# Kernel tuning notes

Measured on AMD Instinct MI355X. Metric: run time of the kernel, lower is better.

## Reference

```python
import jax, jax.numpy as jnp
import numpy as np

N = 20000      # nodes
E = 320000     # directed edges (self-loops added inside reference)
DIN = 128      # input_dim
HID = 64       # hidden_dim
H = 4          # num_heads
B = 16         # graphs in batch
OUT = 1        # output_dim
NEG_SLOPE = 0.2


def setup_inputs() -> dict:
    key = jax.random.key(0)
    ks = jax.random.split(key, 20)
    p = lambda k, shape: (jax.random.normal(k, shape, jnp.float32) * 0.05)
    x = jax.random.normal(ks[0], (N, DIN), jnp.float32)
    edge_index = jax.random.randint(ks[1], (2, E), 0, N, dtype=jnp.int64)
    batch = jnp.sort(jax.random.randint(ks[2], (N,), 0, B, dtype=jnp.int64))
    return {
        "x": x, "edge_index": edge_index, "batch": batch,
        # gat1: DIN -> (H, HID), concat
        "W1": p(ks[3], (DIN, H * HID)), "as1": p(ks[4], (H, HID)), "ad1": p(ks[5], (H, HID)), "b1": jnp.zeros((H * HID,), jnp.float32),
        # gat2: H*HID -> (H, HID), concat
        "W2": p(ks[6], (H * HID, H * HID)), "as2": p(ks[7], (H, HID)), "ad2": p(ks[8], (H, HID)), "b2": jnp.zeros((H * HID,), jnp.float32),
        # gat_out: H*HID -> (1, HID), mean (concat=False)
        "W3": p(ks[9], (H * HID, HID)), "as3": p(ks[10], (1, HID)), "ad3": p(ks[11], (1, HID)), "b3": jnp.zeros((HID,), jnp.float32),
        "wp": p(ks[12], (HID, 1)), "bp": jnp.zeros((1,), jnp.float32),
        "wr": p(ks[13], (HID, OUT)), "br": jnp.zeros((OUT,), jnp.float32),
    }


def _gat_layer(x, W, a_src, a_dst, bias, src, dst, heads, concat):
    n = x.shape[0]
    h = (x @ W).reshape(n, heads, -1)                      # [N,H,C]
    e_src = (h * a_src).sum(-1)                            # [N,H]
    e_dst = (h * a_dst).sum(-1)                            # [N,H]
    e = jax.nn.leaky_relu(e_src[src] + e_dst[dst], NEG_SLOPE)  # [Etot,H]
    # segment softmax over destination node (self-loops guarantee non-empty)
    m = jax.ops.segment_max(e, dst, num_segments=n)
    e = jnp.exp(e - m[dst])
    den = jax.ops.segment_sum(e, dst, num_segments=n)
    alpha = e / den[dst]                                   # [Etot,H]
    out = jax.ops.segment_sum(h[src] * alpha[..., None], dst, num_segments=n)  # [N,H,C]
    out = out.reshape(n, -1) if concat else out.mean(axis=1)
    return out + bias


def reference(x, edge_index, batch, W1, as1, ad1, b1, W2, as2, ad2, b2,
              W3, as3, ad3, b3, wp, bp, wr, br):
    n = x.shape[0]
    loops = jnp.arange(n, dtype=edge_index.dtype)
    src = jnp.concatenate([edge_index[0], loops])
    dst = jnp.concatenate([edge_index[1], loops])

    h = jax.nn.elu(_gat_layer(x, W1, as1, ad1, b1, src, dst, H, True))
    h = jax.nn.elu(_gat_layer(h, W2, as2, ad2, b2, src, dst, H, True))
    h = jax.nn.elu(_gat_layer(h, W3, as3, ad3, b3, src, dst, 1, False))  # [N,HID]

    attn = jax.nn.sigmoid(h @ wp + bp)                     # [N,1]
    hw = h * attn                                          # [N,HID]
    sums = jax.ops.segment_sum(hw, batch, num_segments=B)  # [B,HID]
    counts = jax.ops.segment_sum(jnp.ones((n,), hw.dtype), batch, num_segments=B)
    pooled = sums / jnp.maximum(counts, 1.0)[:, None]
    return pooled @ wr + br                                # [B,OUT]
```

## Files before the change

### kernel.cpp

```cpp
#include <hip/hip_runtime.h>


typedef unsigned short u16;
typedef __attribute__((ext_vector_type(8))) short bf16x8;
typedef __attribute__((ext_vector_type(4))) float f32x4;

__device__ __forceinline__ u16 bf16rn(float x) {
    unsigned u = __float_as_uint(x);
    u += 0x7FFFu + ((u >> 16) & 1u);
    return (u16)(u >> 16);
}
__device__ __forceinline__ float bf16f(u16 h) {
    return __uint_as_float(((unsigned)h) << 16);
}

__device__ __forceinline__ void gload16(const u16* g, u16* l) {
    __builtin_amdgcn_global_load_lds(
        (const __attribute__((address_space(1))) unsigned int*)g,
        (__attribute__((address_space(3))) unsigned int*)l, 16, 0, 0);
}

__global__ void edge_hist_k(const int* __restrict__ ei, int E, int n, int* __restrict__ deg) {
    int i = blockIdx.x * blockDim.x + threadIdx.x;
    if (i >= E + n) return;
    int dst = (i < E) ? ei[E + i] : (i - E);
    atomicAdd(&deg[dst], 1);
}

__global__ void scan_p1_k(const int* __restrict__ deg, int* __restrict__ bsum, int n) {
    __shared__ int red[256];
    int tid = threadIdx.x;
    int i = blockIdx.x * 256 + tid;
    int v = (i < n) ? deg[i] : 0;
    red[tid] = v;
    __syncthreads();
    for (int off = 128; off; off >>= 1) {
        if (tid < off) red[tid] += red[tid + off];
        __syncthreads();
    }
    if (tid == 0) bsum[blockIdx.x] = red[0];
}

__global__ __launch_bounds__(1024) void scan_p2_k(int* __restrict__ bsum, int nb) {
    __shared__ int part[1024];
    int tid = threadIdx.x;
    int v = (tid < nb) ? bsum[tid] : 0;
    part[tid] = v;
    __syncthreads();
    for (int off = 1; off < 1024; off <<= 1) {
        int t = (tid >= off) ? part[tid - off] : 0;
        __syncthreads();
        part[tid] += t;
        __syncthreads();
    }
    if (tid < nb) bsum[tid] = part[tid] - v;
}

__global__ void scan_p3_k(const int* __restrict__ deg, const int* __restrict__ bsum,
                          int* __restrict__ rowptr, int* __restrict__ cursor, int n) {
    __shared__ int part[256];
    int tid = threadIdx.x;
    int i = blockIdx.x * 256 + tid;
    int v = (i < n) ? deg[i] : 0;
    part[tid] = v;
    __syncthreads();
    for (int off = 1; off < 256; off <<= 1) {
        int t = (tid >= off) ? part[tid - off] : 0;
        __syncthreads();
        part[tid] += t;
        __syncthreads();
    }
    int excl = part[tid] - v + bsum[blockIdx.x];
    if (i < n) { rowptr[i] = excl; cursor[i] = excl; }
    if (i == n - 1) rowptr[n] = excl + v;
}

__global__ void edge_scatter_k(const int* __restrict__ ei, int E, int n,
                               int* __restrict__ cursor, int* __restrict__ srcs) {
    int i = blockIdx.x * blockDim.x + threadIdx.x;
    if (i >= E + n) return;
    int src, dst;
    if (i < E) { src = ei[i]; dst = ei[E + i]; }
    else       { src = i - E; dst = src; }
    int pos = atomicAdd(&cursor[dst], 1);
    srcs[pos] = src;
}

__global__ void split_bf16_k(const float* __restrict__ in, u16* __restrict__ hi,
                             u16* __restrict__ lo, int n4) {
    int i = blockIdx.x * 256 + threadIdx.x;
    if (i >= n4) return;
    float4 v = reinterpret_cast<const float4*>(in)[i];
    u16 hx = bf16rn(v.x), hy = bf16rn(v.y), hz = bf16rn(v.z), hw = bf16rn(v.w);
    ushort4 H = make_ushort4(hx, hy, hz, hw);
    ushort4 L = make_ushort4(bf16rn(v.x - bf16f(hx)), bf16rn(v.y - bf16f(hy)),
                             bf16rn(v.z - bf16f(hz)), bf16rn(v.w - bf16f(hw)));
    reinterpret_cast<ushort4*>(hi)[i] = H;
    reinterpret_cast<ushort4*>(lo)[i] = L;
}

__global__ void splitT_bf16_k(const float* __restrict__ W, u16* __restrict__ thi,
                              u16* __restrict__ tlo, int K, int Nn) {
    int idx = blockIdx.x * 256 + threadIdx.x;
    if (idx >= K * Nn) return;
    int k = idx / Nn, nn = idx - k * Nn;
    float v = W[idx];
    u16 h = bf16rn(v);
    u16 l = bf16rn(v - bf16f(h));
    thi[(size_t)nn * K + k] = h;
    tlo[(size_t)nn * K + k] = l;
}

template <int NF>
__global__ __launch_bounds__(256) void gemm_lds_k(
        const u16* __restrict__ Ahi, const u16* __restrict__ Alo,
        const u16* __restrict__ Bthi, const u16* __restrict__ Btlo,
        float* __restrict__ C,
        const float* __restrict__ a_src, const float* __restrict__ a_dst,
        float* __restrict__ esrc, float* __restrict__ edst,
        int M, int Nn, int K) {
    __shared__ u16 Ah[2][4][64 * 8];
    __shared__ u16 Al[2][4][64 * 8];
    const int mb = (M + 63) >> 6;
    const int mi = blockIdx.x % mb;
    const int ni = blockIdx.x / mb;
    const int m0 = mi * 64;
    const int n0 = ni * (NF * 64);
    const int tid = threadIdx.x;
    const int wv = tid >> 6;
    const int lane = tid & 63;
    const int rr = lane & 15;
    const int kg = lane >> 4;

    int srow = m0 + lane; if (srow > M - 1) srow = M - 1;
    const u16* sh = Ahi + (size_t)srow * K + wv * 8;
    const u16* sl = Alo + (size_t)srow * K + wv * 8;

    const u16* pbh[NF];
    const u16* pbl[NF];
#pragma unroll
    for (int nf = 0; nf < NF; ++nf) {
        int col = n0 + (wv * NF + nf) * 16 + rr;
        pbh[nf] = Bthi + (size_t)col * K + kg * 8;
        pbl[nf] = Btlo + (size_t)col * K + kg * 8;
    }

    f32x4 acc[4][NF];
#pragma unroll
    for (int mf = 0; mf < 4; ++mf)
#pragma unroll
        for (int nf = 0; nf < NF; ++nf) acc[mf][nf] = (f32x4){0.f, 0.f, 0.f, 0.f};

    bf16x8 bhc[NF], blc[NF], bhn[NF], bln[NF];
#pragma unroll
    for (int nf = 0; nf < NF; ++nf) {
        bhc[nf] = *reinterpret_cast<const bf16x8*>(pbh[nf]);
        blc[nf] = *reinterpret_cast<const bf16x8*>(pbl[nf]);
    }
    gload16(sh, &Ah[0][wv][0]);
    gload16(sl, &Al[0][wv][0]);
    __syncthreads();

    const int NT = K >> 5;
    for (int t = 0; t < NT; ++t) {
        const int cur = t & 1;
        if (t + 1 < NT) {
            const int kc = (t + 1) << 5;
#pragma unroll
            for (int nf = 0; nf < NF; ++nf) {
                bhn[nf] = *reinterpret_cast<const bf16x8*>(pbh[nf] + kc);
                bln[nf] = *reinterpret_cast<const bf16x8*>(pbl[nf] + kc);
            }
            gload16(sh + kc, &Ah[cur ^ 1][wv][0]);
            gload16(sl + kc, &Al[cur ^ 1][wv][0]);
        }
        bf16x8 ah[4], al[4];
#pragma unroll
        for (int mf = 0; mf < 4; ++mf) {
            ah[mf] = *reinterpret_cast<const bf16x8*>(&Ah[cur][kg][(mf * 16 + rr) * 8]);
            al[mf] = *reinterpret_cast<const bf16x8*>(&Al[cur][kg][(mf * 16 + rr) * 8]);
        }
#pragma unroll
        for (int mf = 0; mf < 4; ++mf)
#pragma unroll
            for (int nf = 0; nf < NF; ++nf) {
                acc[mf][nf] = __builtin_amdgcn_mfma_f32_16x16x32_bf16(ah[mf], bhc[nf], acc[mf][nf], 0, 0, 0);
                acc[mf][nf] = __builtin_amdgcn_mfma_f32_16x16x32_bf16(ah[mf], blc[nf], acc[mf][nf], 0, 0, 0);
                acc[mf][nf] = __builtin_amdgcn_mfma_f32_16x16x32_bf16(al[mf], bhc[nf], acc[mf][nf], 0, 0, 0);
            }
#pragma unroll
        for (int nf = 0; nf < NF; ++nf) { bhc[nf] = bhn[nf]; blc[nf] = bln[nf]; }
        __syncthreads();
    }

#pragma unroll
    for (int mf = 0; mf < 4; ++mf)
#pragma unroll
        for (int nf = 0; nf < NF; ++nf) {
            int col = n0 + (wv * NF + nf) * 16 + rr;
            float* cb = C + ((size_t)(col >> 6) * M) * 64 + (col & 63);
#pragma unroll
            for (int rg = 0; rg < 4; ++rg) {
                int row = m0 + mf * 16 + kg * 4 + rg;
                if (row < M) cb[(size_t)row * 64] = acc[mf][nf][rg];
            }
        }

    float asv[NF], adv[NF];
#pragma unroll
    for (int nf = 0; nf < NF; ++nf) {
        int col = n0 + (wv * NF + nf) * 16 + rr;
        asv[nf] = a_src[col];
        adv[nf] = a_dst[col];
    }
    float ps[4][4], pd[4][4];
#pragma unroll
    for (int mf = 0; mf < 4; ++mf)
#pragma unroll
        for (int rg = 0; rg < 4; ++rg) {
            float s = 0.f, dvv = 0.f;
#pragma unroll
            for (int nf = 0; nf < NF; ++nf) {
                s = fmaf(acc[mf][nf][rg], asv[nf], s);
                dvv = fmaf(acc[mf][nf][rg], adv[nf], dvv);
            }
#pragma unroll
            for (int off = 1; off < 16; off <<= 1) {
                s += __shfl_xor(s, off);
                dvv += __shfl_xor(dvv, off);
            }
            ps[mf][rg] = s;
            pd[mf][rg] = dvv;
        }
    float* sm_src = (float*)&Ah[0][0][0];
    float* sm_dst = sm_src + 256;
    if (rr == 0) {
#pragma unroll
        for (int mf = 0; mf < 4; ++mf)
#pragma unroll
            for (int rg = 0; rg < 4; ++rg) {
                int rl = mf * 16 + kg * 4 + rg;
                sm_src[wv * 64 + rl] = ps[mf][rg];
                sm_dst[wv * 64 + rl] = pd[mf][rg];
            }
    }
    __syncthreads();
    if (tid < 64) {
        int row = m0 + tid;
        if (row < M) {
            const int HTOT = Nn >> 6;
            constexpr int WPH = 4 / NF;
#pragma unroll
            for (int hl = 0; hl < NF; ++hl) {
                float es = 0.f, edv = 0.f;
#pragma unroll
                for (int w = 0; w < WPH; ++w) {
                    es += sm_src[(hl * WPH + w) * 64 + tid];
                    edv += sm_dst[(hl * WPH + w) * 64 + tid];
                }
                int hg = ni * NF + hl;
                esrc[(size_t)row * HTOT + hg] = es;
                edst[(size_t)row * HTOT + hg] = edv;
            }
        }
    }
}

__global__ __launch_bounds__(256) void gat_aggregate_hm_k(
        const float* __restrict__ hm, const float* __restrict__ esrc,
        const float* __restrict__ edst, const int* __restrict__ rowptr,
        const int* __restrict__ srcs, const float* __restrict__ bias,
        u16* __restrict__ ghi, u16* __restrict__ glo, int n) {
    __shared__ int2 swb[4][64];
    int wv = threadIdx.x >> 6;
    int d = blockIdx.x * 4 + wv;
    int lane = threadIdx.x & 63;
    int hh = blockIdx.y;
    if (d >= n) return;
    const float* hbase = hm + (size_t)hh * n * 64;
    const int es = lane >> 4;
    const int cq = lane & 15;
    int2* swv = swb[wv];
    float ed = edst[d * 4 + hh];
    int lo = rowptr[d], hi = rowptr[d + 1];
    float4 acc = make_float4(0.f, 0.f, 0.f, 0.f);
    float den = 0.f;
    for (int base = lo; base < hi; base += 64) {
        int cnt = min(64, hi - base);
        int idx = base + lane;
        int s = srcs[(idx < hi) ? idx : lo];
        float e = esrc[s * 4 + hh] + ed;
        e = (e >= 0.f) ? e : 0.2f * e;
        float w = (lane < cnt) ? __expf(e) : 0.f;
        float ws = w;
#pragma unroll
        for (int off = 1; off < 64; off <<= 1) ws += __shfl_xor(ws, off);
        den += ws;
        swv[lane] = make_int2(s, __float_as_int(w));
        auto ROW = [&](int2 sv) -> float4 {
            return *reinterpret_cast<const float4*>(&hbase[(size_t)sv.x * 64 + cq * 4]);
        };
        int2 s0 = swv[es], s1 = swv[4 + es], s2 = swv[8 + es], s3 = swv[12 + es];
        float4 p0 = ROW(s0), p1 = ROW(s1), p2 = ROW(s2), p3 = ROW(s3);
        for (int j = 0; j < cnt; j += 16) {
            int2 t0 = s0, t1 = s1, t2 = s2, t3 = s3;
            float4 q0 = p0, q1 = p1, q2 = p2, q3 = p3;
            s0 = swv[(j + 16 + es) & 63];
            s1 = swv[(j + 20 + es) & 63];
            s2 = swv[(j + 24 + es) & 63];
            s3 = swv[(j + 28 + es) & 63];
            p0 = ROW(s0); p1 = ROW(s1); p2 = ROW(s2); p3 = ROW(s3);
            float w0 = __int_as_float(t0.y), w1 = __int_as_float(t1.y);
            float w2 = __int_as_float(t2.y), w3 = __int_as_float(t3.y);
            acc.x = fmaf(w0, q0.x, acc.x); acc.y = fmaf(w0, q0.y, acc.y);
            acc.z = fmaf(w0, q0.z, acc.z); acc.w = fmaf(w0, q0.w, acc.w);
            acc.x = fmaf(w1, q1.x, acc.x); acc.y = fmaf(w1, q1.y, acc.y);
            acc.z = fmaf(w1, q1.z, acc.z); acc.w = fmaf(w1, q1.w, acc.w);
            acc.x = fmaf(w2, q2.x, acc.x); acc.y = fmaf(w2, q2.y, acc.y);
            acc.z = fmaf(w2, q2.z, acc.z); acc.w = fmaf(w2, q2.w, acc.w);
            acc.x = fmaf(w3, q3.x, acc.x); acc.y = fmaf(w3, q3.y, acc.y);
            acc.z = fmaf(w3, q3.z, acc.z); acc.w = fmaf(w3, q3.w, acc.w);
        }
    }
    acc.x += __shfl_xor(acc.x, 16); acc.x += __shfl_xor(acc.x, 32);
    acc.y += __shfl_xor(acc.y, 16); acc.y += __shfl_xor(acc.y, 32);
    acc.z += __shfl_xor(acc.z, 16); acc.z += __shfl_xor(acc.z, 32);
    acc.w += __shfl_xor(acc.w, 16); acc.w += __shfl_xor(acc.w, 32);
    if (es == 0) {
        int c0 = hh * 64 + cq * 4;
        float inv = 1.f / den;
        float4 bv = *reinterpret_cast<const float4*>(&bias[c0]);
        float4 o;
        o.x = acc.x * inv + bv.x;
        o.y = acc.y * inv + bv.y;
        o.z = acc.z * inv + bv.z;
        o.w = acc.w * inv + bv.w;
        o.x = (o.x > 0.f) ? o.x : expm1f(o.x);
        o.y = (o.y > 0.f) ? o.y : expm1f(o.y);
        o.z = (o.z > 0.f) ? o.z : expm1f(o.z);
        o.w = (o.w > 0.f) ? o.w : expm1f(o.w);
        u16 hx = bf16rn(o.x), hy = bf16rn(o.y), hz = bf16rn(o.z), hw = bf16rn(o.w);
        ushort4 H = make_ushort4(hx, hy, hz, hw);
        ushort4 L = make_ushort4(bf16rn(o.x - bf16f(hx)), bf16rn(o.y - bf16f(hy)),
                                 bf16rn(o.z - bf16f(hz)), bf16rn(o.w - bf16f(hw)));
        *reinterpret_cast<ushort4*>(&ghi[(size_t)d * 256 + c0]) = H;
        *reinterpret_cast<ushort4*>(&glo[(size_t)d * 256 + c0]) = L;
    }
}

__global__ __launch_bounds__(256) void gat_aggregate1_attn_k(
        const float* __restrict__ hin, const float* __restrict__ esrc,
        const float* __restrict__ edst, const int* __restrict__ rowptr,
        const int* __restrict__ srcs, const float* __restrict__ bias,
        const float* __restrict__ wp, const float* __restrict__ bp,
        float* __restrict__ gout, float* __restrict__ attn, int n) {
    __shared__ int2 swb[4][64];
    int wv = threadIdx.x >> 6;
    int d = blockIdx.x * 4 + wv;
    int lane = threadIdx.x & 63;
    if (d >= n) return;
    const int es = lane >> 4;
    const int cq = lane & 15;
    int2* swv = swb[wv];
    float ed = edst[d];
    int lo = rowptr[d], hi = rowptr[d + 1];
    float4 acc = make_float4(0.f, 0.f, 0.f, 0.f);
    float den = 0.f;
    for (int base = lo; base < hi; base += 64) {
        int cnt = min(64, hi - base);
        int idx = base + lane;
        int s = srcs[(idx < hi) ? idx : lo];
        float e = esrc[s] + ed;
        e = (e >= 0.f) ? e : 0.2f * e;
        float w = (lane < cnt) ? __expf(e) : 0.f;
        float ws = w;
#pragma unroll
        for (int off = 1; off < 64; off <<= 1) ws += __shfl_xor(ws, off);
        den += ws;
        swv[lane] = make_int2(s, __float_as_int(w));
        auto ROW = [&](int2 sv) -> float4 {
            return *reinterpret_cast<const float4*>(&hin[(size_t)sv.x * 64 + cq * 4]);
        };
        int2 s0 = swv[es], s1 = swv[4 + es], s2 = swv[8 + es], s3 = swv[12 + es];
        float4 p0 = ROW(s0), p1 = ROW(s1), p2 = ROW(s2), p3 = ROW(s3);
        for (int j = 0; j < cnt; j += 16) {
            int2 t0 = s0, t1 = s1, t2 = s2, t3 = s3;
            float4 q0 = p0, q1 = p1, q2 = p2, q3 = p3;
            s0 = swv[(j + 16 + es) & 63];
            s1 = swv[(j + 20 + es) & 63];
            s2 = swv[(j + 24 + es) & 63];
            s3 = swv[(j + 28 + es) & 63];
            p0 = ROW(s0); p1 = ROW(s1); p2 = ROW(s2); p3 = ROW(s3);
            float w0 = __int_as_float(t0.y), w1 = __int_as_float(t1.y);
            float w2 = __int_as_float(t2.y), w3 = __int_as_float(t3.y);
            acc.x = fmaf(w0, q0.x, acc.x); acc.y = fmaf(w0, q0.y, acc.y);
            acc.z = fmaf(w0, q0.z, acc.z); acc.w = fmaf(w0, q0.w, acc.w);
            acc.x = fmaf(w1, q1.x, acc.x); acc.y = fmaf(w1, q1.y, acc.y);
            acc.z = fmaf(w1, q1.z, acc.z); acc.w = fmaf(w1, q1.w, acc.w);
            acc.x = fmaf(w2, q2.x, acc.x); acc.y = fmaf(w2, q2.y, acc.y);
            acc.z = fmaf(w2, q2.z, acc.z); acc.w = fmaf(w2, q2.w, acc.w);
            acc.x = fmaf(w3, q3.x, acc.x); acc.y = fmaf(w3, q3.y, acc.y);
            acc.z = fmaf(w3, q3.z, acc.z); acc.w = fmaf(w3, q3.w, acc.w);
        }
    }
    acc.x += __shfl_xor(acc.x, 16); acc.x += __shfl_xor(acc.x, 32);
    acc.y += __shfl_xor(acc.y, 16); acc.y += __shfl_xor(acc.y, 32);
    acc.z += __shfl_xor(acc.z, 16); acc.z += __shfl_xor(acc.z, 32);
    acc.w += __shfl_xor(acc.w, 16); acc.w += __shfl_xor(acc.w, 32);
    int c0 = cq * 4;
    float inv = 1.f / den;
    float4 bv = *reinterpret_cast<const float4*>(&bias[c0]);
    float4 o;
    o.x = acc.x * inv + bv.x;
    o.y = acc.y * inv + bv.y;
    o.z = acc.z * inv + bv.z;
    o.w = acc.w * inv + bv.w;
    o.x = (o.x > 0.f) ? o.x : expm1f(o.x);
    o.y = (o.y > 0.f) ? o.y : expm1f(o.y);
    o.z = (o.z > 0.f) ? o.z : expm1f(o.z);
    o.w = (o.w > 0.f) ? o.w : expm1f(o.w);
    if (es == 0)
        *reinterpret_cast<float4*>(&gout[(size_t)d * 64 + c0]) = o;
    float4 wv4 = *reinterpret_cast<const float4*>(&wp[c0]);
    float v = o.x * wv4.x + o.y * wv4.y + o.z * wv4.z + o.w * wv4.w;
#pragma unroll
    for (int off = 1; off < 16; off <<= 1) v += __shfl_xor(v, off);
    if (lane == 0) attn[d] = 1.f / (1.f + __expf(-(v + bp[0])));
}

__global__ void pool_partial_k(const float* __restrict__ g3, const float* __restrict__ attn,
                               const int* __restrict__ batch, int n, float* __restrict__ sums) {
    int wid = blockIdx.x * (blockDim.x >> 6) + (threadIdx.x >> 6);
    int lane = threadIdx.x & 63;
    int nwaves = gridDim.x * (blockDim.x >> 6);
    int per = (n + nwaves - 1) / nwaves;
    int i0 = wid * per;
    int i1 = i0 + per;
    if (i1 > n) i1 = n;
    if (i0 >= i1) return;
    int cur = batch[i0];
    float acc = 0.f;
    for (int i = i0; i < i1; ++i) {
        int b = batch[i];
        if (b != cur) {
            atomicAdd(&sums[cur * 64 + lane], acc);
            acc = 0.f;
            cur = b;
        }
        acc += g3[(size_t)i * 64 + lane] * attn[i];
    }
    atomicAdd(&sums[cur * 64 + lane], acc);
}

__global__ void regress_k(const float* __restrict__ sums, const int* __restrict__ batch, int n,
                          const float* __restrict__ wr, const float* __restrict__ br,
                          float* __restrict__ out, int B) {
    int b = threadIdx.x >> 6;
    int lane = threadIdx.x & 63;
    if (b >= B) return;
    int lo = 0, hi = n;
    while (lo < hi) { int mid = (lo + hi) >> 1; if (batch[mid] < b) lo = mid + 1; else hi = mid; }
    int seg_lo = lo;
    lo = 0; hi = n;
    while (lo < hi) { int mid = (lo + hi) >> 1; if (batch[mid] < b + 1) lo = mid + 1; else hi = mid; }
    float cnt = (float)(lo - seg_lo);
    if (cnt < 1.f) cnt = 1.f;
    float v = (sums[b * 64 + lane] / cnt) * wr[lane];
#pragma unroll
    for (int off = 32; off; off >>= 1) v += __shfl_xor(v, off);
    if (lane == 0) out[b] = v + br[0];
}

extern "C" void kernel_launch(void* const* d_in, const int* in_sizes, int n_in,
                              void* d_out, int out_size, void* d_ws, size_t ws_size,
                              hipStream_t stream) {
    const float* x   = (const float*)d_in[0];
    const int*   ei  = (const int*)d_in[1];
    const int*   bat = (const int*)d_in[2];
    const float* W1  = (const float*)d_in[3];
    const float* as1 = (const float*)d_in[4];
    const float* ad1 = (const float*)d_in[5];
    const float* b1  = (const float*)d_in[6];
    const float* W2  = (const float*)d_in[7];
    const float* as2 = (const float*)d_in[8];
    const float* ad2 = (const float*)d_in[9];
    const float* b2  = (const float*)d_in[10];
    const float* W3  = (const float*)d_in[11];
    const float* as3 = (const float*)d_in[12];
    const float* ad3 = (const float*)d_in[13];
    const float* b3  = (const float*)d_in[14];
    const float* wp  = (const float*)d_in[15];
    const float* bp  = (const float*)d_in[16];
    const float* wr  = (const float*)d_in[17];
    const float* br  = (const float*)d_in[18];
    float* out = (float*)d_out;

    const int N    = in_sizes[2];
    const int E    = in_sizes[1] / 2;
    const int DIN  = in_sizes[0] / N;
    const int Etot = E + N;
    const int Bc   = out_size;

    char* ws = (char*)d_ws;
    size_t off = 0;
    auto alloc = [&](size_t bytes) {
        void* p = ws + off;
        off = (off + bytes + 255) & ~(size_t)255;
        return p;
    };
    int*   deg    = (int*)alloc((size_t)N * 4);
    int*   rowptr = (int*)alloc((size_t)(N + 1) * 4);
    int*   cursor = (int*)alloc((size_t)N * 4);
    int*   bsum   = (int*)alloc((size_t)1024 * 4);
    int*   srcs   = (int*)alloc((size_t)Etot * 4);
    float* bufA   = (float*)alloc((size_t)N * 256 * 4);
    u16*   Ahi    = (u16*)alloc((size_t)N * 256 * 2);
    u16*   Alo    = (u16*)alloc((size_t)N * 256 * 2);
    float* h3     = (float*)alloc((size_t)N * 64 * 4);
    float* g3     = (float*)alloc((size_t)N * 64 * 4);
    float* esrc   = (float*)alloc((size_t)N * 4 * 4);
    float* edst   = (float*)alloc((size_t)N * 4 * 4);
    float* attn   = (float*)alloc((size_t)N * 4);
    float* sums   = (float*)alloc((size_t)Bc * 64 * 4);
    u16*   w1hi   = (u16*)alloc((size_t)256 * DIN * 2);
    u16*   w1lo   = (u16*)alloc((size_t)256 * DIN * 2);
    u16*   w2hi   = (u16*)alloc((size_t)256 * 256 * 2);
    u16*   w2lo   = (u16*)alloc((size_t)256 * 256 * 2);
    u16*   w3hi   = (u16*)alloc((size_t)64 * 256 * 2);
    u16*   w3lo   = (u16*)alloc((size_t)64 * 256 * 2);
    (void)ws_size;

    hipMemsetAsync(deg, 0, (size_t)N * 4, stream);
    int eb = (Etot + 255) / 256;
    int nb = (N + 255) / 256;
    edge_hist_k<<<eb, 256, 0, stream>>>(ei, E, N, deg);
    scan_p1_k<<<nb, 256, 0, stream>>>(deg, bsum, N);
    scan_p2_k<<<1, 1024, 0, stream>>>(bsum, nb);
    scan_p3_k<<<nb, 256, 0, stream>>>(deg, bsum, rowptr, cursor, N);
    edge_scatter_k<<<eb, 256, 0, stream>>>(ei, E, N, cursor, srcs);

    splitT_bf16_k<<<(DIN * 256 + 255) / 256, 256, 0, stream>>>(W1, w1hi, w1lo, DIN, 256);
    splitT_bf16_k<<<(256 * 256 + 255) / 256, 256, 0, stream>>>(W2, w2hi, w2lo, 256, 256);
    splitT_bf16_k<<<(256 * 64 + 255) / 256, 256, 0, stream>>>(W3, w3hi, w3lo, 256, 64);
    split_bf16_k<<<(N * DIN / 4 + 255) / 256, 256, 0, stream>>>(x, Ahi, Alo, N * DIN / 4);

    const int mb = (N + 63) / 64;
    int nb4 = (N + 3) / 4;
    dim3 agg_grid(nb4, 4);

    gemm_lds_k<2><<<mb * 2, 256, 0, stream>>>(Ahi, Alo, w1hi, w1lo, bufA, as1, ad1, esrc, edst, N, 256, DIN);
    gat_aggregate_hm_k<<<agg_grid, 256, 0, stream>>>(bufA, esrc, edst, rowptr, srcs, b1, Ahi, Alo, N);

    gemm_lds_k<2><<<mb * 2, 256, 0, stream>>>(Ahi, Alo, w2hi, w2lo, bufA, as2, ad2, esrc, edst, N, 256, 256);
    gat_aggregate_hm_k<<<agg_grid, 256, 0, stream>>>(bufA, esrc, edst, rowptr, srcs, b2, Ahi, Alo, N);

    gemm_lds_k<1><<<mb, 256, 0, stream>>>(Ahi, Alo, w3hi, w3lo, h3, as3, ad3, esrc, edst, N, 64, 256);
    gat_aggregate1_attn_k<<<nb4, 256, 0, stream>>>(h3, esrc, edst, rowptr, srcs, b3, wp, bp, g3, attn, N);

    hipMemsetAsync(sums, 0, (size_t)Bc * 64 * 4, stream);
    pool_partial_k<<<256, 256, 0, stream>>>(g3, attn, bat, N, sums);
    regress_k<<<1, 1024, 0, stream>>>(sums, bat, N, wr, br, out, Bc);
}
```

Before: 251.0 us.

## Precompute attention edge weights in separate kernels and widen aggregation gather parallelism

Moves the softmax numerator and denominator computation out of the aggregation kernels into new per-edge weight kernels that write weights and per-node denominators to a workspace buffer. The multi-head aggregation grid now splits each head's 64 channels into two halves, so each wave loads 8 neighbor rows at once instead of a 4-deep software pipeline. The single-head aggregation issues 8 row loads per batch, with predicated unrolled steps. This aims to increase memory-level parallelism in the gathers and to remove redundant exp and reduction work per channel block. In exchange it adds extra kernel launches, an extra edge-sized buffer that is written and read back, and srcs/weights re-read twice per head in the split grid.

After: 306.5 us. +22.1%, slower.

```diff
diff --git a/kernel.cpp b/kernel.cpp
--- a/kernel.cpp
+++ b/kernel.cpp
@@ -266,69 +266,116 @@
     }
 }
 
+__global__ __launch_bounds__(256) void edge_w4_k(
+        const float* __restrict__ esrc, const float* __restrict__ edst,
+        const int* __restrict__ rowptr, const int* __restrict__ srcs,
+        float* __restrict__ wbuf, float* __restrict__ den, int n, int Etot) {
+    int wv = threadIdx.x >> 6;
+    int d = blockIdx.x * 4 + wv;
+    int lane = threadIdx.x & 63;
+    if (d >= n) return;
+    int hh = lane >> 4, jj = lane & 15;
+    float ed = edst[d * 4 + hh];
+    int lo = rowptr[d], hi = rowptr[d + 1];
+    float dacc = 0.f;
+    for (int base = lo; base < hi; base += 16) {
+        int idx = base + jj;
+        bool val = idx < hi;
+        int s = srcs[val ? idx : lo];
+        float e = esrc[s * 4 + hh] + ed;
+        e = (e >= 0.f) ? e : 0.2f * e;
+        float w = val ? __expf(e) : 0.f;
+        if (val) wbuf[(size_t)hh * Etot + idx] = w;
+        dacc += w;
+    }
+#pragma unroll
+    for (int off = 1; off < 16; off <<= 1) dacc += __shfl_xor(dacc, off);
+    if (jj == 0) den[d * 4 + hh] = dacc;
+}
+
+__global__ __launch_bounds__(256) void edge_w1_k(
+        const float* __restrict__ esrc, const float* __restrict__ edst,
+        const int* __restrict__ rowptr, const int* __restrict__ srcs,
+        float* __restrict__ wbuf, float* __restrict__ den, int n) {
+    int wv = threadIdx.x >> 6;
+    int d = blockIdx.x * 4 + wv;
+    int lane = threadIdx.x & 63;
+    if (d >= n) return;
+    float ed = edst[d];
+    int lo = rowptr[d], hi = rowptr[d + 1];
+    float dacc = 0.f;
+    for (int base = lo; base < hi; base += 64) {
+        int idx = base + lane;
+        bool val = idx < hi;
+        int s = srcs[val ? idx : lo];
+        float e = esrc[s] + ed;
+        e = (e >= 0.f) ? e : 0.2f * e;
+        float w = val ? __expf(e) : 0.f;
+        if (val) wbuf[idx] = w;
+        dacc += w;
+    }
+#pragma unroll
+    for (int off = 1; off < 64; off <<= 1) dacc += __shfl_xor(dacc, off);
+    if (lane == 0) den[d] = dacc;
+}
+
+#define HM_STEP(K, T, R)                                                       \
+    if (cnt > 8 * K) {                                                         \
+        float wk = __int_as_float(T.y);                                        \
+        acc.x = fmaf(wk, R.x, acc.x); acc.y = fmaf(wk, R.y, acc.y);            \
+        acc.z = fmaf(wk, R.z, acc.z); acc.w = fmaf(wk, R.w, acc.w);            \
+    }
+
 __global__ __launch_bounds__(256) void gat_aggregate_hm_k(
-        const float* __restrict__ hm, const float* __restrict__ esrc,
-        const float* __restrict__ edst, const int* __restrict__ rowptr,
+        const float* __restrict__ hm, const float* __restrict__ wbuf,
+        const float* __restrict__ den4, const int* __restrict__ rowptr,
         const int* __restrict__ srcs, const float* __restrict__ bias,
-        u16* __restrict__ ghi, u16* __restrict__ glo, int n) {
+        u16* __restrict__ ghi, u16* __restrict__ glo, int n, int Etot) {
     __shared__ int2 swb[4][64];
     int wv = threadIdx.x >> 6;
     int d = blockIdx.x * 4 + wv;
     int lane = threadIdx.x & 63;
-    int hh = blockIdx.y;
+    int hh = blockIdx.y >> 1;
+    int ch = blockIdx.y & 1;
     if (d >= n) return;
-    const float* hbase = hm + (size_t)hh * n * 64;
-    const int es = lane >> 4;
-    const int cq = lane & 15;
+    const float* hbase = hm + (size_t)hh * n * 64 + ch * 32;
+    const int es = lane >> 3;
+    const int cq = lane & 7;
     int2* swv = swb[wv];
-    float ed = edst[d * 4 + hh];
     int lo = rowptr[d], hi = rowptr[d + 1];
     float4 acc = make_float4(0.f, 0.f, 0.f, 0.f);
-    float den = 0.f;
     for (int base = lo; base < hi; base += 64) {
         int cnt = min(64, hi - base);
         int idx = base + lane;
-        int s = srcs[(idx < hi) ? idx : lo];
-        float e = esrc[s * 4 + hh] + ed;
-        e = (e >= 0.f) ? e : 0.2f * e;
-        float w = (lane < cnt) ? __expf(e) : 0.f;
-        float ws = w;
-#pragma unroll
-        for (int off = 1; off < 64; off <<= 1) ws += __shfl_xor(ws, off);
-        den += ws;
+        bool val = lane < cnt;
+        int s = srcs[val ? idx : lo];
+        float w = val ? wbuf[(size_t)hh * Etot + idx] : 0.f;
         swv[lane] = make_int2(s, __float_as_int(w));
-        auto ROW = [&](int2 sv) -> float4 {
-            return *reinterpret_cast<const float4*>(&hbase[(size_t)sv.x * 64 + cq * 4]);
+        auto ROW = [&](int2 t) -> float4 {
+            return *reinterpret_cast<const float4*>(&hbase[(size_t)t.x * 64 + cq * 4]);
         };
-        int2 s0 = swv[es], s1 = swv[4 + es], s2 = swv[8 + es], s3 = swv[12 + es];
-        float4 p0 = ROW(s0), p1 = ROW(s1), p2 = ROW(s2), p3 = ROW(s3);
-        for (int j = 0; j < cnt; j += 16) {
-            int2 t0 = s0, t1 = s1, t2 = s2, t3 = s3;
-            float4 q0 = p0, q1 = p1, q2 = p2, q3 = p3;
-            s0 = swv[(j + 16 + es) & 63];
-            s1 = swv[(j + 20 + es) & 63];
-            s2 = swv[(j + 24 + es) & 63];
-            s3 = swv[(j + 28 + es) & 63];
-            p0 = ROW(s0); p1 = ROW(s1); p2 = ROW(s2); p3 = ROW(s3);
-            float w0 = __int_as_float(t0.y), w1 = __int_as_float(t1.y);
-            float w2 = __int_as_float(t2.y), w3 = __int_as_float(t3.y);
-            acc.x = fmaf(w0, q0.x, acc.x); acc.y = fmaf(w0, q0.y, acc.y);
-            acc.z = fmaf(w0, q0.z, acc.z); acc.w = fmaf(w0, q0.w, acc.w);
-            acc.x = fmaf(w1, q1.x, acc.x); acc.y = fmaf(w1, q1.y, acc.y);
-            acc.z = fmaf(w1, q1.z, acc.z); acc.w = fmaf(w1, q1.w, acc.w);
-            acc.x = fmaf(w2, q2.x, acc.x); acc.y = fmaf(w2, q2.y, acc.y);
-            acc.z = fmaf(w2, q2.z, acc.z); acc.w = fmaf(w2, q2.w, acc.w);
-            acc.x = fmaf(w3, q3.x, acc.x); acc.y = fmaf(w3, q3.y, acc.y);
-            acc.z = fmaf(w3, q3.z, acc.z); acc.w = fmaf(w3, q3.w, acc.w);
-        }
-    }
-    acc.x += __shfl_xor(acc.x, 16); acc.x += __shfl_xor(acc.x, 32);
-    acc.y += __shfl_xor(acc.y, 16); acc.y += __shfl_xor(acc.y, 32);
-    acc.z += __shfl_xor(acc.z, 16); acc.z += __shfl_xor(acc.z, 32);
-    acc.w += __shfl_xor(acc.w, 16); acc.w += __shfl_xor(acc.w, 32);
+        float4 z = make_float4(0.f, 0.f, 0.f, 0.f);
+        int2 zi = make_int2(0, 0);
+        int2 t0 = zi, t1 = zi, t2 = zi, t3 = zi, t4 = zi, t5 = zi, t6 = zi, t7 = zi;
+        float4 r0 = z, r1 = z, r2 = z, r3 = z, r4 = z, r5 = z, r6 = z, r7 = z;
+        t0 = swv[es];           r0 = ROW(t0);
+        if (cnt >  8) { t1 = swv[ 8 + es]; r1 = ROW(t1); }
+        if (cnt > 16) { t2 = swv[16 + es]; r2 = ROW(t2); }
+        if (cnt > 24) { t3 = swv[24 + es]; r3 = ROW(t3); }
+        if (cnt > 32) { t4 = swv[32 + es]; r4 = ROW(t4); }
+        if (cnt > 40) { t5 = swv[40 + es]; r5 = ROW(t5); }
+        if (cnt > 48) { t6 = swv[48 + es]; r6 = ROW(t6); }
+        if (cnt > 56) { t7 = swv[56 + es]; r7 = ROW(t7); }
+        HM_STEP(0, t0, r0) HM_STEP(1, t1, r1) HM_STEP(2, t2, r2) HM_STEP(3, t3, r3)
+        HM_STEP(4, t4, r4) HM_STEP(5, t5, r5) HM_STEP(6, t6, r6) HM_STEP(7, t7, r7)
+    }
+    acc.x += __shfl_xor(acc.x, 8); acc.x += __shfl_xor(acc.x, 16); acc.x += __shfl_xor(acc.x, 32);
+    acc.y += __shfl_xor(acc.y, 8); acc.y += __shfl_xor(acc.y, 16); acc.y += __shfl_xor(acc.y, 32);
+    acc.z += __shfl_xor(acc.z, 8); acc.z += __shfl_xor(acc.z, 16); acc.z += __shfl_xor(acc.z, 32);
+    acc.w += __shfl_xor(acc.w, 8); acc.w += __shfl_xor(acc.w, 16); acc.w += __shfl_xor(acc.w, 32);
     if (es == 0) {
-        int c0 = hh * 64 + cq * 4;
-        float inv = 1.f / den;
+        int c0 = hh * 64 + ch * 32 + cq * 4;
+        float inv = 1.f / den4[d * 4 + hh];
         float4 bv = *reinterpret_cast<const float4*>(&bias[c0]);
         float4 o;
         o.x = acc.x * inv + bv.x;
@@ -348,9 +395,16 @@
     }
 }
 
+#define A1_STEP(K, T, R)                                                       \
+    if (cnt > 4 * K) {                                                         \
+        float wk = __int_as_float(T.y);                                        \
+        acc.x = fmaf(wk, R.x, acc.x); acc.y = fmaf(wk, R.y, acc.y);            \
+        acc.z = fmaf(wk, R.z, acc.z); acc.w = fmaf(wk, R.w, acc.w);            \
+    }
+
 __global__ __launch_bounds__(256) void gat_aggregate1_attn_k(
-        const float* __restrict__ hin, const float* __restrict__ esrc,
-        const float* __restrict__ edst, const int* __restrict__ rowptr,
+        const float* __restrict__ hin, const float* __restrict__ wbuf,
+        const float* __restrict__ den1, const int* __restrict__ rowptr,
         const int* __restrict__ srcs, const float* __restrict__ bias,
         const float* __restrict__ wp, const float* __restrict__ bp,
         float* __restrict__ gout, float* __restrict__ attn, int n) {
@@ -362,45 +416,43 @@
     const int es = lane >> 4;
     const int cq = lane & 15;
     int2* swv = swb[wv];
-    float ed = edst[d];
     int lo = rowptr[d], hi = rowptr[d + 1];
     float4 acc = make_float4(0.f, 0.f, 0.f, 0.f);
-    float den = 0.f;
     for (int base = lo; base < hi; base += 64) {
         int cnt = min(64, hi - base);
         int idx = base + lane;
-        int s = srcs[(idx < hi) ? idx : lo];
-        float e = esrc[s] + ed;
-        e = (e >= 0.f) ? e : 0.2f * e;
-        float w = (lane < cnt) ? __expf(e) : 0.f;
-        float ws = w;
-#pragma unroll
-        for (int off = 1; off < 64; off <<= 1) ws += __shfl_xor(ws, off);
-        den += ws;
+        bool val = lane < cnt;
+        int s = srcs[val ? idx : lo];
+        float w = val ? wbuf[idx] : 0.f;
         swv[lane] = make_int2(s, __float_as_int(w));
-        auto ROW = [&](int2 sv) -> float4 {
-            return *reinterpret_cast<const float4*>(&hin[(size_t)sv.x * 64 + cq * 4]);
+        auto ROW = [&](int2 t) -> float4 {
+            return *reinterpret_cast<const float4*>(&hin[(size_t)t.x * 64 + cq * 4]);
         };
-        int2 s0 = swv[es], s1 = swv[4 + es], s2 = swv[8 + es], s3 = swv[12 + es];
-        float4 p0 = ROW(s0), p1 = ROW(s1), p2 = ROW(s2), p3 = ROW(s3);
-        for (int j = 0; j < cnt; j += 16) {
-            int2 t0 = s0, t1 = s1, t2 = s2, t3 = s3;
-            float4 q0 = p0, q1 = p1, q2 = p2, q3 = p3;
-            s0 = swv[(j + 16 + es) & 63];
-            s1 = swv[(j + 20 + es) & 63];
-            s2 = swv[(j + 24 + es) & 63];
-            s3 = swv[(j + 28 + es) & 63];
-            p0 = ROW(s0); p1 = ROW(s1); p2 = ROW(s2); p3 = ROW(s3);
-            float w0 = __int_as_float(t0.y), w1 = __int_as_float(t1.y);
-            float w2 = __int_as_float(t2.y), w3 = __int_as_float(t3.y);
-            acc.x = fmaf(w0, q0.x, acc.x); acc.y = fmaf(w0, q0.y, acc.y);
-            acc.z = fmaf(w0, q0.z, acc.z); acc.w = fmaf(w0, q0.w, acc.w);
-            acc.x = fmaf(w1, q1.x, acc.x); acc.y = fmaf(w1, q1.y, acc.y);
-            acc.z = fmaf(w1, q1.z, acc.z); acc.w = fmaf(w1, q1.w, acc.w);
-            acc.x = fmaf(w2, q2.x, acc.x); acc.y = fmaf(w2, q2.y, acc.y);
-            acc.z = fmaf(w2, q2.z, acc.z); acc.w = fmaf(w2, q2.w, acc.w);
-            acc.x = fmaf(w3, q3.x, acc.x); acc.y = fmaf(w3, q3.y, acc.y);
-            acc.z = fmaf(w3, q3.z, acc.z); acc.w = fmaf(w3, q3.w, acc.w);
+        float4 z = make_float4(0.f, 0.f, 0.f, 0.f);
+        int2 zi = make_int2(0, 0);
+        int2 t0 = zi, t1 = zi, t2 = zi, t3 = zi, t4 = zi, t5 = zi, t6 = zi, t7 = zi;
+        float4 r0 = z, r1 = z, r2 = z, r3 = z, r4 = z, r5 = z, r6 = z, r7 = z;
+        t0 = swv[es];           r0 = ROW(t0);
+        if (cnt >  4) { t1 = swv[ 4 + es]; r1 = ROW(t1); }
+        if (cnt >  8) { t2 = swv[ 8 + es]; r2 = ROW(t2); }
+        if (cnt > 12) { t3 = swv[12 + es]; r3 = ROW(t3); }
+        if (cnt > 16) { t4 = swv[16 + es]; r4 = ROW(t4); }
+        if (cnt > 20) { t5 = swv[20 + es]; r5 = ROW(t5); }
+        if (cnt > 24) { t6 = swv[24 + es]; r6 = ROW(t6); }
+        if (cnt > 28) { t7 = swv[28 + es]; r7 = ROW(t7); }
+        A1_STEP(0, t0, r0) A1_STEP(1, t1, r1) A1_STEP(2, t2, r2) A1_STEP(3, t3, r3)
+        A1_STEP(4, t4, r4) A1_STEP(5, t5, r5) A1_STEP(6, t6, r6) A1_STEP(7, t7, r7)
+        if (cnt > 32) {
+            t0 = swv[32 + es];             r0 = ROW(t0);
+            if (cnt > 36) { t1 = swv[36 + es]; r1 = ROW(t1); }
+            if (cnt > 40) { t2 = swv[40 + es]; r2 = ROW(t2); }
+            if (cnt > 44) { t3 = swv[44 + es]; r3 = ROW(t3); }
+            if (cnt > 48) { t4 = swv[48 + es]; r4 = ROW(t4); }
+            if (cnt > 52) { t5 = swv[52 + es]; r5 = ROW(t5); }
+            if (cnt > 56) { t6 = swv[56 + es]; r6 = ROW(t6); }
+            if (cnt > 60) { t7 = swv[60 + es]; r7 = ROW(t7); }
+            A1_STEP(8, t0, r0)  A1_STEP(9, t1, r1)  A1_STEP(10, t2, r2) A1_STEP(11, t3, r3)
+            A1_STEP(12, t4, r4) A1_STEP(13, t5, r5) A1_STEP(14, t6, r6) A1_STEP(15, t7, r7)
         }
     }
     acc.x += __shfl_xor(acc.x, 16); acc.x += __shfl_xor(acc.x, 32);
@@ -408,7 +460,7 @@
     acc.z += __shfl_xor(acc.z, 16); acc.z += __shfl_xor(acc.z, 32);
     acc.w += __shfl_xor(acc.w, 16); acc.w += __shfl_xor(acc.w, 32);
     int c0 = cq * 4;
-    float inv = 1.f / den;
+    float inv = 1.f / den1[d];
     float4 bv = *reinterpret_cast<const float4*>(&bias[c0]);
     float4 o;
     o.x = acc.x * inv + bv.x;
@@ -520,6 +572,8 @@
     float* g3     = (float*)alloc((size_t)N * 64 * 4);
     float* esrc   = (float*)alloc((size_t)N * 4 * 4);
     float* edst   = (float*)alloc((size_t)N * 4 * 4);
+    float* wbuf   = (float*)alloc((size_t)Etot * 4 * 4);
+    float* den4   = (float*)alloc((size_t)N * 4 * 4);
     float* attn   = (float*)alloc((size_t)N * 4);
     float* sums   = (float*)alloc((size_t)Bc * 64 * 4);
     u16*   w1hi   = (u16*)alloc((size_t)256 * DIN * 2);
@@ -546,16 +600,19 @@
 
     const int mb = (N + 63) / 64;
     int nb4 = (N + 3) / 4;
-    dim3 agg_grid(nb4, 4);
+    dim3 agg_grid(nb4, 8);
 
     gemm_lds_k<2><<<mb * 2, 256, 0, stream>>>(Ahi, Alo, w1hi, w1lo, bufA, as1, ad1, esrc, edst, N, 256, DIN);
-    gat_aggregate_hm_k<<<agg_grid, 256, 0, stream>>>(bufA, esrc, edst, rowptr, srcs, b1, Ahi, Alo, N);
+    edge_w4_k<<<nb4, 256, 0, stream>>>(esrc, edst, rowptr, srcs, wbuf, den4, N, Etot);
+    gat_aggregate_hm_k<<<agg_grid, 256, 0, stream>>>(bufA, wbuf, den4, rowptr, srcs, b1, Ahi, Alo, N, Etot);
 
     gemm_lds_k<2><<<mb * 2, 256, 0, stream>>>(Ahi, Alo, w2hi, w2lo, bufA, as2, ad2, esrc, edst, N, 256, 256);
-    gat_aggregate_hm_k<<<agg_grid, 256, 0, stream>>>(bufA, esrc, edst, rowptr, srcs, b2, Ahi, Alo, N);
+    edge_w4_k<<<nb4, 256, 0, stream>>>(esrc, edst, rowptr, srcs, wbuf, den4, N, Etot);
+    gat_aggregate_hm_k<<<agg_grid, 256, 0, stream>>>(bufA, wbuf, den4, rowptr, srcs, b2, Ahi, Alo, N, Etot);
 
     gemm_lds_k<1><<<mb, 256, 0, stream>>>(Ahi, Alo, w3hi, w3lo, h3, as3, ad3, esrc, edst, N, 64, 256);
-    gat_aggregate1_attn_k<<<nb4, 256, 0, stream>>>(h3, esrc, edst, rowptr, srcs, b3, wp, bp, g3, attn, N);
+    edge_w1_k<<<nb4, 256, 0, stream>>>(esrc, edst, rowptr, srcs, wbuf, den4, N);
+    gat_aggregate1_attn_k<<<nb4, 256, 0, stream>>>(h3, wbuf, den4, rowptr, srcs, b3, wp, bp, g3, attn, N);
 
     hipMemsetAsync(sums, 0, (size_t)Bc * 64 * 4, stream);
     pool_partial_k<<<256, 256, 0, stream>>>(g3, attn, bat, N, sums);
```
